# Kernel optimization log

Measured on AMD Instinct MI355X. Metric: run time of the kernel, lower is better.

Reference implementation:

```python
import jax, jax.numpy as jnp
import numpy as np

B, T, I, H, O = 64, 2048, 16, 256, 1


def _gru_layer(x, Wih, Whh, bih, bhh):
    # x: [B, T, in]; Wih: [3H, in]; Whh: [3H, H]
    xg = jnp.einsum('bti,gi->btg', x, Wih) + bih  # [B, T, 3H] precomputed input gates

    def step(h, xg_t):
        gh = h @ Whh.T + bhh  # [B, 3H]
        xr, xz, xn = jnp.split(xg_t, 3, axis=-1)
        hr, hz, hn = jnp.split(gh, 3, axis=-1)
        r = jax.nn.sigmoid(xr + hr)
        z = jax.nn.sigmoid(xz + hz)
        n = jnp.tanh(xn + r * hn)
        h_new = (1.0 - z) * n + z * h
        return h_new, h_new

    h0 = jnp.zeros((x.shape[0], Whh.shape[1]), dtype=x.dtype)
    _, hs = jax.lax.scan(step, h0, jnp.swapaxes(xg, 0, 1))  # [T, B, H]
    return jnp.swapaxes(hs, 0, 1)  # [B, T, H]


def setup_inputs() -> dict:
    key = jax.random.key(0)
    ks = jax.random.split(key, 8)

    def xavier(k, shape):
        fan_out, fan_in = shape
        lim = float(np.sqrt(6.0 / (fan_in + fan_out)))
        return jax.random.uniform(k, shape, jnp.float32, -lim, lim)

    return {
        'x': jax.random.normal(ks[0], (B, T, I), jnp.float32),
        'Wih0': xavier(ks[1], (3 * H, I)),
        'Whh0': xavier(ks[2], (3 * H, H)),
        'bih0': jnp.zeros((3 * H,), jnp.float32),
        'bhh0': jnp.zeros((3 * H,), jnp.float32),
        'Wih1': xavier(ks[3], (3 * H, H)),
        'Whh1': xavier(ks[4], (3 * H, H)),
        'bih1': jnp.zeros((3 * H,), jnp.float32),
        'bhh1': jnp.zeros((3 * H,), jnp.float32),
        'W1': xavier(ks[5], (H, H)),
        'b1': jnp.zeros((H,), jnp.float32),
        'W2': xavier(ks[6], (O, H)),
        'b2': jnp.zeros((O,), jnp.float32),
    }


def reference(x, Wih0, Whh0, bih0, bhh0, Wih1, Whh1, bih1, bhh1, W1, b1, W2, b2):
    h1 = _gru_layer(x, Wih0, Whh0, bih0, bhh0)    # layer 0: [B, T, H]
    h2 = _gru_layer(h1, Wih1, Whh1, bih1, bhh1)   # layer 1: [B, T, H]
    r = jax.nn.relu(jnp.einsum('bth,oh->bto', h2, W1) + b1)
    out = jnp.einsum('bth,oh->bto', r, W2) + b2
    return jax.nn.relu(out)  # final relu in forward, [B, T, O]
```

## Files before the change

kernel.cpp:

```cpp
#include <hip/hip_runtime.h>
#include <hip/hip_fp16.h>
#include <stdint.h>

#define B_ 64
#define T_ 2048
#define I_ 16
#define H_ 256
#define G_ 768

#define REC_SMEM 132160

typedef _Float16 f16;
typedef _Float16 half2_t __attribute__((ext_vector_type(2)));
typedef uint32_t u32x4 __attribute__((ext_vector_type(4)));

__device__ __forceinline__ float fast_rcp(float x) {
#if __has_builtin(__builtin_amdgcn_rcpf)
    return __builtin_amdgcn_rcpf(x);
#else
    return 1.0f / x;
#endif
}
__device__ __forceinline__ float sigmoid_f(float x) {
    return fast_rcp(1.0f + __expf(-x));
}
__device__ __forceinline__ float tanh_f(float x) {
    float e = __expf(2.0f * x);
    return 1.0f - 2.0f * fast_rcp(e + 1.0f);
}

__device__ __forceinline__ float fdot2(uint32_t a, uint32_t b, float c) {
#if __has_builtin(__builtin_amdgcn_fdot2)
    return __builtin_amdgcn_fdot2(__builtin_bit_cast(half2_t, a),
                                  __builtin_bit_cast(half2_t, b), c, false);
#else
    half2_t ha = __builtin_bit_cast(half2_t, a), hb = __builtin_bit_cast(half2_t, b);
    return c + (float)ha.x * (float)hb.x + (float)ha.y * (float)hb.y;
#endif
}
__device__ __forceinline__ float dot_u4(u32x4 w, u32x4 h, float acc) {
    acc = fdot2(w.x, h.x, acc);
    acc = fdot2(w.y, h.y, acc);
    acc = fdot2(w.z, h.z, acc);
    acc = fdot2(w.w, h.w, acc);
    return acc;
}

__global__ __launch_bounds__(256) void cvt_weights(const float* __restrict__ whh0,
                                                   const float* __restrict__ whh1,
                                                   const float* __restrict__ wih1,
                                                   const float* __restrict__ w1,
                                                   uint32_t* __restrict__ out) {
    int idx = blockIdx.x * 256 + threadIdx.x;
    if (idx >= 327680) return;
    const float* s;
    if (idx < 196608) {
        const float* w = (idx < 98304) ? whh0 : whh1;
        int lidx = (idx < 98304) ? idx : idx - 98304;
        int u4 = lidx >> 2, d = lidx & 3;
        int P = u4 >> 9, t = u4 & 511;
        int j = t >> 1, hf = t & 1;
        int gate = P >> 4, u = P & 15;
        int row = gate * 256 + j;
        int halfoff = hf * 128 + u * 8;
        s = w + (size_t)row * 256 + halfoff + d * 2;
    } else if (idx < 294912) {
        int local = idx - 196608;
        int u4 = local >> 2, d = local & 3;
        int k8 = u4 / 768, g = u4 - k8 * 768;
        s = wih1 + (size_t)g * 256 + k8 * 8 + d * 2;
    } else {
        int local = idx - 294912;
        int u4 = local >> 2, d = local & 3;
        int k8 = u4 >> 8, g = u4 & 255;
        s = w1 + (size_t)g * 256 + k8 * 8 + d * 2;
    }
    half2_t h;
    h.x = (f16)s[0];
    h.y = (f16)s[1];
    out[idx] = __builtin_bit_cast(uint32_t, h);
}


__device__ __forceinline__ void xg0_body(const float* __restrict__ x,
        const float* __restrict__ wih0, const float* __restrict__ bih0,
        float* __restrict__ xg, int t0, int C, int blk, char* smem) {
    float (*xs)[16] = (float(*)[16])smem;
    int tid = threadIdx.x;
    int m0 = blk * 64;
    if (tid < 256) {
        int r = tid >> 2, c4 = (tid & 3) * 4;
        int m = m0 + r;
        int b = m / C, tl = m - b * C;
        float4 v = *(const float4*)(x + (size_t)(b * T_ + t0 + tl) * I_ + c4);
        *(float4*)&xs[r][c4] = v;
    }
    __syncthreads();
    for (int g = tid; g < G_; g += 512) {
        const float4* wr = (const float4*)(wih0 + (size_t)g * I_);
        float4 w0 = wr[0], w1 = wr[1], w2 = wr[2], w3 = wr[3];
        float bias = bih0[g];
        float* outp = xg + (size_t)m0 * G_ + g;
        for (int m = 0; m < 64; ++m) {
            const float4* xr4 = (const float4*)xs[m];
            float4 a0 = xr4[0], a1 = xr4[1], a2 = xr4[2], a3 = xr4[3];
            float acc = bias;
            acc += a0.x*w0.x + a0.y*w0.y + a0.z*w0.z + a0.w*w0.w;
            acc += a1.x*w1.x + a1.y*w1.y + a1.z*w1.z + a1.w*w1.w;
            acc += a2.x*w2.x + a2.y*w2.y + a2.z*w2.z + a2.w*w2.w;
            acc += a3.x*w3.x + a3.y*w3.y + a3.z*w3.z + a3.w*w3.w;
            outp[(size_t)m * G_] = acc;
        }
    }
}

__device__ __forceinline__ void xg1_body(const f16* __restrict__ h1,
        const uint32_t* __restrict__ wih1T, const float* __restrict__ bih1,
        float* __restrict__ xg, int C, int lgC, int blk, char* smem) {
    u32x4 (*hs)[32] = (u32x4(*)[32])smem;
    int tid = threadIdx.x;
    int m0 = (blk & (C - 1)) * 64;
    int gbase = (blk >> lgC) * 256;
    const u32x4* hsrc = (const u32x4*)h1 + (size_t)m0 * 32;
    #pragma unroll
    for (int it = 0; it < 4; ++it) {
        int o = tid + it * 512;
        hs[o >> 5][o & 31] = hsrc[o];
    }
    __syncthreads();
    int gg = tid & 31, mg = tid >> 5;
    const u32x4* wt = (const u32x4*)wih1T;
    float acc[8][4];
    #pragma unroll
    for (int i = 0; i < 8; ++i)
        #pragma unroll
        for (int r = 0; r < 4; ++r) acc[i][r] = 0.0f;
    for (int k8 = 0; k8 < 32; ++k8) {
        u32x4 w[8], h[4];
        #pragma unroll
        for (int i = 0; i < 8; ++i) w[i] = wt[(size_t)k8 * 768 + gbase + gg + 32 * i];
        #pragma unroll
        for (int r = 0; r < 4; ++r) h[r] = hs[mg * 4 + r][k8];
        #pragma unroll
        for (int i = 0; i < 8; ++i)
            #pragma unroll
            for (int r = 0; r < 4; ++r)
                acc[i][r] = dot_u4(w[i], h[r], acc[i][r]);
    }
    #pragma unroll
    for (int i = 0; i < 8; ++i) {
        int g = gbase + gg + 32 * i;
        float bias = bih1[g];
        #pragma unroll
        for (int r = 0; r < 4; ++r)
            xg[(size_t)(m0 + mg * 4 + r) * G_ + g] = acc[i][r] + bias;
    }
}

__device__ __forceinline__ void reg_body(const f16* __restrict__ h2,
        const uint32_t* __restrict__ w1T, const float* __restrict__ b1,
        const float* __restrict__ w2, const float* __restrict__ b2,
        float* __restrict__ out, int t0, int C, int lgC, int blk, char* smem) {
    u32x4 (*hs)[32] = (u32x4(*)[32])smem;
    float (*red)[4] = (float(*)[4])(smem + 32768);
    int tid = threadIdx.x;
    int m0 = blk * 64;
    const u32x4* hsrc = (const u32x4*)h2 + (size_t)m0 * 32;
    #pragma unroll
    for (int it = 0; it < 4; ++it) {
        int o = tid + it * 512;
        hs[o >> 5][o & 31] = hsrc[o];
    }
    __syncthreads();
    int gg = tid & 31, mg = tid >> 5;
    const u32x4* wt = (const u32x4*)w1T;
    float acc[8][4];
    #pragma unroll
    for (int i = 0; i < 8; ++i)
        #pragma unroll
        for (int r = 0; r < 4; ++r) acc[i][r] = 0.0f;
    for (int k8 = 0; k8 < 32; ++k8) {
        u32x4 w[8], h[4];
        #pragma unroll
        for (int i = 0; i < 8; ++i) w[i] = wt[(size_t)k8 * 256 + gg + 32 * i];
        #pragma unroll
        for (int r = 0; r < 4; ++r) h[r] = hs[mg * 4 + r][k8];
        #pragma unroll
        for (int i = 0; i < 8; ++i)
            #pragma unroll
            for (int r = 0; r < 4; ++r)
                acc[i][r] = dot_u4(w[i], h[r], acc[i][r]);
    }
    float pv[4] = {0, 0, 0, 0};
    #pragma unroll
    for (int i = 0; i < 8; ++i) {
        int g = gg + 32 * i;
        float bias = b1[g], w2g = w2[g];
        #pragma unroll
        for (int r = 0; r < 4; ++r)
            pv[r] += w2g * fmaxf(acc[i][r] + bias, 0.0f);
    }
    #pragma unroll
    for (int r = 0; r < 4; ++r) {
        pv[r] += __shfl_xor(pv[r], 1, 64);
        pv[r] += __shfl_xor(pv[r], 2, 64);
        pv[r] += __shfl_xor(pv[r], 4, 64);
        pv[r] += __shfl_xor(pv[r], 8, 64);
        pv[r] += __shfl_xor(pv[r], 16, 64);
    }
    if (gg == 0) {
        #pragma unroll
        for (int r = 0; r < 4; ++r) red[mg][r] = pv[r];
    }
    __syncthreads();
    if (tid < 64) {
        int m = m0 + tid;
        float v = fmaxf(red[tid >> 2][tid & 3] + b2[0], 0.0f);
        int b = m >> lgC, tl = m & (C - 1);
        out[(size_t)b * T_ + t0 + tl] = v;
    }
}

__device__ __forceinline__ void rec_body(const uint32_t* __restrict__ whh,
        const float* __restrict__ bhh, const float* __restrict__ xg,
        f16* __restrict__ hout, float* __restrict__ state,
        int b, int C, char* smem) {
    int tid = threadIdx.x;
    int j = tid >> 1, hf = tid & 1;
    const u32x4* wb = (const u32x4*)whh;
    u32x4* wlds = (u32x4*)smem;
    u32x4 (*hq)[2][17] = (u32x4(*)[2][17])(smem + 131072);

    #pragma unroll
    for (int s = 0; s < 16; ++s)
        wlds[s * 512 + tid] = wb[(32 + s) * 512 + tid];

    u32x4 R4  = wb[ 4 * 512 + tid], R5  = wb[ 5 * 512 + tid];
    u32x4 R6  = wb[ 6 * 512 + tid], R7  = wb[ 7 * 512 + tid];
    u32x4 R8  = wb[ 8 * 512 + tid], R9  = wb[ 9 * 512 + tid];
    u32x4 R10 = wb[10 * 512 + tid], R11 = wb[11 * 512 + tid];
    u32x4 R12 = wb[12 * 512 + tid], R13 = wb[13 * 512 + tid];
    u32x4 R14 = wb[14 * 512 + tid], R15 = wb[15 * 512 + tid];

    float h_old = 0.0f, bhr = 0.0f, bhz = 0.0f, bhn = 0.0f;
    if (hf == 0) {
        h_old = state[b * 256 + j];
        bhr = bhh[j]; bhz = bhh[256 + j]; bhn = bhh[512 + j];
        ((f16*)&hq[0][j >> 7][0])[j & 127] = (f16)h_old;
    }
    __syncthreads();

    const float* xgt = xg + (size_t)b * C * G_;
    f16* hob = hout + (size_t)b * C * H_;
    const u32x4* nl = wlds + tid;

    for (int tl = 0; tl < C; ++tl) {
        int p = tl & 1;
        float xr = 0, xz = 0, xn = 0;
        if (hf == 0) { xr = xgt[j]; xz = xgt[256 + j]; xn = xgt[512 + j]; }

        u32x4 S0 = wb[0 * 512 + tid], S1 = wb[1 * 512 + tid];
        u32x4 S2 = wb[2 * 512 + tid], S3 = wb[3 * 512 + tid];

        const u32x4* hp = &hq[p][hf][0];
        float aR = 0.0f, aZ = 0.0f, aN = 0.0f;

#define STEPU(u, WR) { u32x4 hv = hp[u]; \
        u32x4 wz = wb[(16 + (u)) * 512 + tid]; \
        u32x4 wn = nl[(u) * 512]; \
        aR = dot_u4(WR, hv, aR); \
        aZ = dot_u4(wz, hv, aZ); \
        aN = dot_u4(wn, hv, aN); }

        STEPU(0, S0)  STEPU(1, S1)  STEPU(2, S2)  STEPU(3, S3)
        STEPU(4, R4)  STEPU(5, R5)  STEPU(6, R6)  STEPU(7, R7)
        STEPU(8, R8)  STEPU(9, R9)  STEPU(10, R10) STEPU(11, R11)
        STEPU(12, R12) STEPU(13, R13) STEPU(14, R14) STEPU(15, R15)
#undef STEPU

        aR += __shfl_xor(aR, 1, 64);
        aZ += __shfl_xor(aZ, 1, 64);
        aN += __shfl_xor(aN, 1, 64);

        if (hf == 0) {
            float r = sigmoid_f(xr + aR + bhr);
            float z = sigmoid_f(xz + aZ + bhz);
            float n = tanh_f(xn + r * (aN + bhn));
            h_old = z * (h_old - n) + n;
            f16 hh = (f16)h_old;
            hob[(size_t)tl * H_ + j] = hh;
            ((f16*)&hq[p ^ 1][j >> 7][0])[j & 127] = hh;
        }
        __syncthreads();
        xgt += G_;
    }
    if (hf == 0) state[b * 256 + j] = h_old;
}

__global__ __launch_bounds__(512) void fused_step(int i, int nC, int C, int lgC,
        const float* __restrict__ x,
        const float* __restrict__ wih0, const float* __restrict__ bih0,
        const uint32_t* __restrict__ whh0, const float* __restrict__ bhh0,
        const uint32_t* __restrict__ whh1, const float* __restrict__ bhh1,
        const uint32_t* __restrict__ wih1T, const float* __restrict__ bih1,
        const uint32_t* __restrict__ w1T, const float* __restrict__ b1,
        const float* __restrict__ w2, const float* __restrict__ b2,
        float* __restrict__ xg0a, float* __restrict__ xg0b,
        float* __restrict__ xg1a, float* __restrict__ xg1b,
        f16* __restrict__ h1a, f16* __restrict__ h1b,
        f16* __restrict__ h2a, f16* __restrict__ h2b,
        float* __restrict__ st0, float* __restrict__ st1,
        float* __restrict__ out) {
    extern __shared__ __align__(16) char smem[];
    int blk = blockIdx.x;
    if (blk < 64) {
        if (i >= nC) return;
        rec_body(whh0, bhh0, (i & 1) ? xg0b : xg0a,
                 (i & 1) ? h1b : h1a, st0, blk, C, smem);
    } else if (blk < 128) {
        int c = i - 2;
        if (c < 0 || c >= nC) return;
        rec_body(whh1, bhh1, (c & 1) ? xg1b : xg1a,
                 (c & 1) ? h2b : h2a, st1, blk - 64, C, smem);
    } else if (blk < 128 + C) {
        int c = i + 1;
        if (c >= nC) return;
        xg0_body(x, wih0, bih0, (c & 1) ? xg0b : xg0a, c * C, C, blk - 128, smem);
    } else if (blk < 128 + 4 * C) {
        int c = i - 1;
        if (c < 0 || c >= nC) return;
        xg1_body((c & 1) ? h1b : h1a, wih1T, bih1,
                 (c & 1) ? xg1b : xg1a, C, lgC, blk - 128 - C, smem);
    } else {
        int c = i - 3;
        if (c < 0 || c >= nC) return;
        reg_body((c & 1) ? h2b : h2a, w1T, b1, w2, b2, out, c * C, C, lgC,
                 blk - 128 - 4 * C, smem);
    }
}

__global__ __launch_bounds__(512) void xg0_stand(const float* __restrict__ x,
        const float* __restrict__ wih0, const float* __restrict__ bih0,
        float* __restrict__ xg, int t0, int C) {
    __shared__ __align__(16) char smem[4096];
    xg0_body(x, wih0, bih0, xg, t0, C, blockIdx.x, smem);
}

extern "C" void kernel_launch(void* const* d_in, const int* in_sizes, int n_in,
                              void* d_out, int out_size, void* d_ws, size_t ws_size,
                              hipStream_t stream) {
    const float* x    = (const float*)d_in[0];
    const float* Wih0 = (const float*)d_in[1];
    const float* Whh0 = (const float*)d_in[2];
    const float* bih0 = (const float*)d_in[3];
    const float* bhh0 = (const float*)d_in[4];
    const float* Wih1 = (const float*)d_in[5];
    const float* Whh1 = (const float*)d_in[6];
    const float* bih1 = (const float*)d_in[7];
    const float* bhh1 = (const float*)d_in[8];
    const float* W1   = (const float*)d_in[9];
    const float* b1   = (const float*)d_in[10];
    const float* W2   = (const float*)d_in[11];
    const float* b2   = (const float*)d_in[12];
    float* out = (float*)d_out;

    hipFuncSetAttribute(reinterpret_cast<const void*>(fused_step),
                        hipFuncAttributeMaxDynamicSharedMemorySize, REC_SMEM);

    char* ws = (char*)d_ws;
    uint32_t* wcvt = (uint32_t*)ws;
    const uint32_t* whh0c = wcvt;
    const uint32_t* whh1c = wcvt + 98304;
    const uint32_t* wih1T = wcvt + 196608;
    const uint32_t* w1T   = wcvt + 294912;
    float* state0 = (float*)(ws + 1310720);
    float* state1 = (float*)(ws + 1310720 + 65536);
    size_t fixed = 1310720 + 2 * 65536;

    int C = 512;
    while (C > 32 && fixed + (size_t)C * 917504 > ws_size) C >>= 1;
    int lgC = 0; while ((1 << lgC) < C) lgC++;
    int nC = T_ / C;

    char* p = ws + fixed;
    float* xg0_buf[2]; float* xg1_buf[2];
    f16* h1_buf[2]; f16* h2_buf[2];
    xg0_buf[0] = (float*)p;  p += (size_t)C * 196608;
    xg0_buf[1] = (float*)p;  p += (size_t)C * 196608;
    xg1_buf[0] = (float*)p;  p += (size_t)C * 196608;
    xg1_buf[1] = (float*)p;  p += (size_t)C * 196608;
    h1_buf[0] = (f16*)p;     p += (size_t)C * 32768;
    h1_buf[1] = (f16*)p;     p += (size_t)C * 32768;
    h2_buf[0] = (f16*)p;     p += (size_t)C * 32768;
    h2_buf[1] = (f16*)p;

    cvt_weights<<<1280, 256, 0, stream>>>(Whh0, Whh1, Wih1, W1, wcvt);
    hipMemsetAsync(state0, 0, 2 * 65536, stream);
    xg0_stand<<<C, 512, 0, stream>>>(x, Wih0, bih0, xg0_buf[0], 0, C);

    for (int i = 0; i <= nC + 2; ++i) {
        fused_step<<<128 + 5 * C, 512, REC_SMEM, stream>>>(i, nC, C, lgC,
            x, Wih0, bih0, whh0c, bhh0, whh1c, bhh1, wih1T, bih1, w1T, b1, W2, b2,
            xg0_buf[0], xg0_buf[1], xg1_buf[0], xg1_buf[1],
            h1_buf[0], h1_buf[1], h2_buf[0], h2_buf[1],
            state0, state1, out);
    }
}
```

Baseline: 3.022 ms.

## Rebalance recurrent weight residency across registers, LDS and global; shrink chunk size

```diff
diff --git a/kernel.cpp b/kernel.cpp
--- a/kernel.cpp
+++ b/kernel.cpp
@@ -8,7 +8,7 @@
 #define H_ 256
 #define G_ 768
 
-#define REC_SMEM 132160
+#define REC_SMEM 140352
 
 typedef _Float16 f16;
 typedef _Float16 half2_t __attribute__((ext_vector_type(2)));
@@ -229,18 +229,22 @@
     int j = tid >> 1, hf = tid & 1;
     const u32x4* wb = (const u32x4*)whh;
     u32x4* wlds = (u32x4*)smem;
-    u32x4 (*hq)[2][17] = (u32x4(*)[2][17])(smem + 131072);
+    u32x4 (*hq)[2][17] = (u32x4(*)[2][17])(smem + 139264);
 
     #pragma unroll
     for (int s = 0; s < 16; ++s)
         wlds[s * 512 + tid] = wb[(32 + s) * 512 + tid];
-
+    wlds[16 * 512 + tid] = wb[18 * 512 + tid];
+
+    u32x4 R0  = wb[ 0 * 512 + tid], R1  = wb[ 1 * 512 + tid];
+    u32x4 R2  = wb[ 2 * 512 + tid], R3  = wb[ 3 * 512 + tid];
     u32x4 R4  = wb[ 4 * 512 + tid], R5  = wb[ 5 * 512 + tid];
     u32x4 R6  = wb[ 6 * 512 + tid], R7  = wb[ 7 * 512 + tid];
     u32x4 R8  = wb[ 8 * 512 + tid], R9  = wb[ 9 * 512 + tid];
     u32x4 R10 = wb[10 * 512 + tid], R11 = wb[11 * 512 + tid];
     u32x4 R12 = wb[12 * 512 + tid], R13 = wb[13 * 512 + tid];
     u32x4 R14 = wb[14 * 512 + tid], R15 = wb[15 * 512 + tid];
+    u32x4 Z0  = wb[16 * 512 + tid], Z1  = wb[17 * 512 + tid];
 
     float h_old = 0.0f, bhr = 0.0f, bhz = 0.0f, bhn = 0.0f;
     if (hf == 0) {
@@ -259,24 +263,35 @@
         float xr = 0, xz = 0, xn = 0;
         if (hf == 0) { xr = xgt[j]; xz = xgt[256 + j]; xn = xgt[512 + j]; }
 
-        u32x4 S0 = wb[0 * 512 + tid], S1 = wb[1 * 512 + tid];
-        u32x4 S2 = wb[2 * 512 + tid], S3 = wb[3 * 512 + tid];
-
         const u32x4* hp = &hq[p][hf][0];
         float aR = 0.0f, aZ = 0.0f, aN = 0.0f;
 
-#define STEPU(u, WR) { u32x4 hv = hp[u]; \
-        u32x4 wz = wb[(16 + (u)) * 512 + tid]; \
-        u32x4 wn = nl[(u) * 512]; \
-        aR = dot_u4(WR, hv, aR); \
-        aZ = dot_u4(wz, hv, aZ); \
-        aN = dot_u4(wn, hv, aN); }
-
-        STEPU(0, S0)  STEPU(1, S1)  STEPU(2, S2)  STEPU(3, S3)
-        STEPU(4, R4)  STEPU(5, R5)  STEPU(6, R6)  STEPU(7, R7)
-        STEPU(8, R8)  STEPU(9, R9)  STEPU(10, R10) STEPU(11, R11)
-        STEPU(12, R12) STEPU(13, R13) STEPU(14, R14) STEPU(15, R15)
-#undef STEPU
+#define PU(u, ZSRC) { u32x4 hv = hp[u]; \
+        aR = dot_u4(R##u, hv, aR); \
+        aN = dot_u4(nl[(u) * 512], hv, aN); \
+        aZ = dot_u4(ZSRC, hv, aZ); }
+
+        u32x4 S3 = wb[19 * 512 + tid], S4 = wb[20 * 512 + tid];
+        u32x4 S5 = wb[21 * 512 + tid], S6 = wb[22 * 512 + tid];
+        u32x4 S7 = wb[23 * 512 + tid], S8 = wb[24 * 512 + tid];
+
+        PU(0, Z0)
+        PU(1, Z1)
+        PU(2, nl[16 * 512])
+        PU(3, S3)  u32x4 S9  = wb[25 * 512 + tid];
+        PU(4, S4)  u32x4 S10 = wb[26 * 512 + tid];
+        PU(5, S5)  u32x4 S11 = wb[27 * 512 + tid];
+        PU(6, S6)  u32x4 S12 = wb[28 * 512 + tid];
+        PU(7, S7)  u32x4 S13 = wb[29 * 512 + tid];
+        PU(8, S8)  u32x4 S14 = wb[30 * 512 + tid];
+        PU(9, S9)  u32x4 S15 = wb[31 * 512 + tid];
+        PU(10, S10)
+        PU(11, S11)
+        PU(12, S12)
+        PU(13, S13)
+        PU(14, S14)
+        PU(15, S15)
+#undef PU
 
         aR += __shfl_xor(aR, 1, 64);
         aZ += __shfl_xor(aZ, 1, 64);
@@ -297,7 +312,9 @@
     if (hf == 0) state[b * 256 + j] = h_old;
 }
 
-__global__ __launch_bounds__(512) void fused_step(int i, int nC, int C, int lgC,
+__global__ __launch_bounds__(512)
+__attribute__((amdgpu_waves_per_eu(2, 2)))
+void fused_step(int i, int nC, int C, int lgC,
         const float* __restrict__ x,
         const float* __restrict__ wih0, const float* __restrict__ bih0,
         const uint32_t* __restrict__ whh0, const float* __restrict__ bhh0,
@@ -377,7 +394,7 @@
     float* state1 = (float*)(ws + 1310720 + 65536);
     size_t fixed = 1310720 + 2 * 65536;
 
-    int C = 512;
+    int C = 128;
     while (C > 32 && fixed + (size_t)C * 917504 > ws_size) C >>= 1;
     int lgC = 0; while ((1 << lgC) < C) lgC++;
     int nC = T_ / C;
```

After: 2.823 ms. 6.6% less time.

## Store reset-gate recurrent weights as 8-bit and rebalance weight placement

Applied to the files above, without the earlier changes.

```diff
diff --git a/kernel.cpp b/kernel.cpp
--- a/kernel.cpp
+++ b/kernel.cpp
@@ -8,11 +8,12 @@
 #define H_ 256
 #define G_ 768
 
-#define REC_SMEM 132160
+#define REC_SMEM 156736
 
 typedef _Float16 f16;
 typedef _Float16 half2_t __attribute__((ext_vector_type(2)));
 typedef uint32_t u32x4 __attribute__((ext_vector_type(4)));
+typedef uint32_t u32x2 __attribute__((ext_vector_type(2)));
 
 __device__ __forceinline__ float fast_rcp(float x) {
 #if __has_builtin(__builtin_amdgcn_rcpf)
@@ -52,33 +53,52 @@
                                                    const float* __restrict__ w1,
                                                    uint32_t* __restrict__ out) {
     int idx = blockIdx.x * 256 + threadIdx.x;
-    if (idx >= 327680) return;
-    const float* s;
-    if (idx < 196608) {
-        const float* w = (idx < 98304) ? whh0 : whh1;
-        int lidx = (idx < 98304) ? idx : idx - 98304;
-        int u4 = lidx >> 2, d = lidx & 3;
-        int P = u4 >> 9, t = u4 & 511;
-        int j = t >> 1, hf = t & 1;
-        int gate = P >> 4, u = P & 15;
-        int row = gate * 256 + j;
-        int halfoff = hf * 128 + u * 8;
-        s = w + (size_t)row * 256 + halfoff + d * 2;
-    } else if (idx < 294912) {
-        int local = idx - 196608;
+    if (idx >= 294912) return;
+    if (idx < 163840) {
+        const float* w = (idx < 81920) ? whh0 : whh1;
+        int l = (idx < 81920) ? idx : idx - 81920;
+        if (l < 65536) {
+            int u4 = l >> 2, d = l & 3;
+            int P = u4 >> 9, t = u4 & 511;
+            int j = t >> 1, hf = t & 1;
+            int row = (P < 16) ? (256 + j) : (512 + j);
+            int u = (P < 16) ? P : P - 16;
+            const float* s = w + (size_t)row * 256 + hf * 128 + u * 8 + d * 2;
+            half2_t h;
+            h.x = (f16)s[0];
+            h.y = (f16)s[1];
+            out[idx] = __builtin_bit_cast(uint32_t, h);
+        } else {
+            int l2 = l - 65536;
+            int P8 = l2 >> 10, wd = l2 & 1023;
+            int t = wd >> 1, piece = wd & 1;
+            int j = t >> 1, hf = t & 1;
+            const float* s = w + (size_t)j * 256 + hf * 128 + P8 * 8 + piece * 4;
+            uint32_t dw = 0;
+            #pragma unroll
+            for (int k = 0; k < 4; ++k) {
+                f16 hh = (f16)s[k];
+                uint16_t hb = __builtin_bit_cast(uint16_t, hh);
+                uint16_t r8 = (uint16_t)((hb + 0x7F + ((hb >> 8) & 1)) >> 8);
+                dw |= (uint32_t)(r8 & 0xFF) << (8 * k);
+            }
+            out[idx] = dw;
+        }
+    } else if (idx < 262144) {
+        int local = idx - 163840;
         int u4 = local >> 2, d = local & 3;
         int k8 = u4 / 768, g = u4 - k8 * 768;
-        s = wih1 + (size_t)g * 256 + k8 * 8 + d * 2;
+        const float* s = wih1 + (size_t)g * 256 + k8 * 8 + d * 2;
+        half2_t h; h.x = (f16)s[0]; h.y = (f16)s[1];
+        out[idx] = __builtin_bit_cast(uint32_t, h);
     } else {
-        int local = idx - 294912;
+        int local = idx - 262144;
         int u4 = local >> 2, d = local & 3;
         int k8 = u4 >> 8, g = u4 & 255;
-        s = w1 + (size_t)g * 256 + k8 * 8 + d * 2;
-    }
-    half2_t h;
-    h.x = (f16)s[0];
-    h.y = (f16)s[1];
-    out[idx] = __builtin_bit_cast(uint32_t, h);
+        const float* s = w1 + (size_t)g * 256 + k8 * 8 + d * 2;
+        half2_t h; h.x = (f16)s[0]; h.y = (f16)s[1];
+        out[idx] = __builtin_bit_cast(uint32_t, h);
+    }
 }
 
 
@@ -228,19 +248,23 @@
     int tid = threadIdx.x;
     int j = tid >> 1, hf = tid & 1;
     const u32x4* wb = (const u32x4*)whh;
+    const u32x2* w8 = (const u32x2*)(whh + 65536);
     u32x4* wlds = (u32x4*)smem;
-    u32x4 (*hq)[2][17] = (u32x4(*)[2][17])(smem + 131072);
+    u32x4 (*hq)[2][17] = (u32x4(*)[2][17])(smem + 155648);
 
     #pragma unroll
     for (int s = 0; s < 16; ++s)
-        wlds[s * 512 + tid] = wb[(32 + s) * 512 + tid];
-
-    u32x4 R4  = wb[ 4 * 512 + tid], R5  = wb[ 5 * 512 + tid];
-    u32x4 R6  = wb[ 6 * 512 + tid], R7  = wb[ 7 * 512 + tid];
-    u32x4 R8  = wb[ 8 * 512 + tid], R9  = wb[ 9 * 512 + tid];
-    u32x4 R10 = wb[10 * 512 + tid], R11 = wb[11 * 512 + tid];
-    u32x4 R12 = wb[12 * 512 + tid], R13 = wb[13 * 512 + tid];
-    u32x4 R14 = wb[14 * 512 + tid], R15 = wb[15 * 512 + tid];
+        wlds[s * 512 + tid] = wb[(16 + s) * 512 + tid];
+    #pragma unroll
+    for (int s = 0; s < 3; ++s)
+        wlds[(16 + s) * 512 + tid] = wb[(12 + s) * 512 + tid];
+
+    u32x4 Z0  = wb[ 0 * 512 + tid], Z1  = wb[ 1 * 512 + tid];
+    u32x4 Z2  = wb[ 2 * 512 + tid], Z3  = wb[ 3 * 512 + tid];
+    u32x4 Z4  = wb[ 4 * 512 + tid], Z5  = wb[ 5 * 512 + tid];
+    u32x4 Z6  = wb[ 6 * 512 + tid], Z7  = wb[ 7 * 512 + tid];
+    u32x4 Z8  = wb[ 8 * 512 + tid], Z9  = wb[ 9 * 512 + tid];
+    u32x4 Z10 = wb[10 * 512 + tid], Z11 = wb[11 * 512 + tid];
 
     float h_old = 0.0f, bhr = 0.0f, bhz = 0.0f, bhn = 0.0f;
     if (hf == 0) {
@@ -256,27 +280,37 @@
 
     for (int tl = 0; tl < C; ++tl) {
         int p = tl & 1;
+        u32x2 F0  = w8[ 0 * 512 + tid], F1  = w8[ 1 * 512 + tid];
+        u32x2 F2  = w8[ 2 * 512 + tid], F3  = w8[ 3 * 512 + tid];
+        u32x2 F4  = w8[ 4 * 512 + tid], F5  = w8[ 5 * 512 + tid];
+        u32x2 F6  = w8[ 6 * 512 + tid], F7  = w8[ 7 * 512 + tid];
+        u32x2 F8  = w8[ 8 * 512 + tid], F9  = w8[ 9 * 512 + tid];
+        u32x2 F10 = w8[10 * 512 + tid], F11 = w8[11 * 512 + tid];
+        u32x2 F12 = w8[12 * 512 + tid], F13 = w8[13 * 512 + tid];
+        u32x2 F14 = w8[14 * 512 + tid], F15 = w8[15 * 512 + tid];
+        u32x4 SZ = wb[15 * 512 + tid];
         float xr = 0, xz = 0, xn = 0;
         if (hf == 0) { xr = xgt[j]; xz = xgt[256 + j]; xn = xgt[512 + j]; }
 
-        u32x4 S0 = wb[0 * 512 + tid], S1 = wb[1 * 512 + tid];
-        u32x4 S2 = wb[2 * 512 + tid], S3 = wb[3 * 512 + tid];
-
         const u32x4* hp = &hq[p][hf][0];
         float aR = 0.0f, aZ = 0.0f, aN = 0.0f;
 
-#define STEPU(u, WR) { u32x4 hv = hp[u]; \
-        u32x4 wz = wb[(16 + (u)) * 512 + tid]; \
-        u32x4 wn = nl[(u) * 512]; \
-        aR = dot_u4(WR, hv, aR); \
-        aZ = dot_u4(wz, hv, aZ); \
-        aN = dot_u4(wn, hv, aN); }
-
-        STEPU(0, S0)  STEPU(1, S1)  STEPU(2, S2)  STEPU(3, S3)
-        STEPU(4, R4)  STEPU(5, R5)  STEPU(6, R6)  STEPU(7, R7)
-        STEPU(8, R8)  STEPU(9, R9)  STEPU(10, R10) STEPU(11, R11)
-        STEPU(12, R12) STEPU(13, R13) STEPU(14, R14) STEPU(15, R15)
-#undef STEPU
+#define PU(u, ZS) { u32x4 hv = hp[u]; \
+        aN = dot_u4(nl[(u) * 512], hv, aN); \
+        aZ = dot_u4(ZS, hv, aZ); \
+        u32x4 wr; \
+        wr.x = __byte_perm(F##u.x, 0u, 0x1404); \
+        wr.y = __byte_perm(F##u.x, 0u, 0x3424); \
+        wr.z = __byte_perm(F##u.y, 0u, 0x1404); \
+        wr.w = __byte_perm(F##u.y, 0u, 0x3424); \
+        aR = dot_u4(wr, hv, aR); }
+
+        PU(0,  Z0)  PU(1,  Z1)  PU(2,  Z2)  PU(3,  Z3)
+        PU(4,  Z4)  PU(5,  Z5)  PU(6,  Z6)  PU(7,  Z7)
+        PU(8,  Z8)  PU(9,  Z9)  PU(10, Z10) PU(11, Z11)
+        PU(12, nl[16 * 512]) PU(13, nl[17 * 512]) PU(14, nl[18 * 512])
+        PU(15, SZ)
+#undef PU
 
         aR += __shfl_xor(aR, 1, 64);
         aZ += __shfl_xor(aZ, 1, 64);
@@ -297,7 +331,9 @@
     if (hf == 0) state[b * 256 + j] = h_old;
 }
 
-__global__ __launch_bounds__(512) void fused_step(int i, int nC, int C, int lgC,
+__global__ __launch_bounds__(512)
+__attribute__((amdgpu_waves_per_eu(2, 2)))
+void fused_step(int i, int nC, int C, int lgC,
         const float* __restrict__ x,
         const float* __restrict__ wih0, const float* __restrict__ bih0,
         const uint32_t* __restrict__ whh0, const float* __restrict__ bhh0,
@@ -370,14 +406,14 @@
     char* ws = (char*)d_ws;
     uint32_t* wcvt = (uint32_t*)ws;
     const uint32_t* whh0c = wcvt;
-    const uint32_t* whh1c = wcvt + 98304;
-    const uint32_t* wih1T = wcvt + 196608;
-    const uint32_t* w1T   = wcvt + 294912;
-    float* state0 = (float*)(ws + 1310720);
-    float* state1 = (float*)(ws + 1310720 + 65536);
-    size_t fixed = 1310720 + 2 * 65536;
-
-    int C = 512;
+    const uint32_t* whh1c = wcvt + 81920;
+    const uint32_t* wih1T = wcvt + 163840;
+    const uint32_t* w1T   = wcvt + 262144;
+    float* state0 = (float*)(ws + 1179648);
+    float* state1 = (float*)(ws + 1179648 + 65536);
+    size_t fixed = 1179648 + 2 * 65536;
+
+    int C = 128;
     while (C > 32 && fixed + (size_t)C * 917504 > ws_size) C >>= 1;
     int lgC = 0; while ((1 << lgC) < C) lgC++;
     int nC = T_ / C;
@@ -394,7 +430,7 @@
     h2_buf[0] = (f16*)p;     p += (size_t)C * 32768;
     h2_buf[1] = (f16*)p;
 
-    cvt_weights<<<1280, 256, 0, stream>>>(Whh0, Whh1, Wih1, W1, wcvt);
+    cvt_weights<<<1152, 256, 0, stream>>>(Whh0, Whh1, Wih1, W1, wcvt);
     hipMemsetAsync(state0, 0, 2 * 65536, stream);
     xg0_stand<<<C, 512, 0, stream>>>(x, Wih0, bih0, xg0_buf[0], 0, C);
 
```

After: 2.788 ms. -7.7%, faster.
